# Kernel optimization log

Hardware: AMD Instinct MI355X
Metric: run time of the kernel (lower is better)

## Reference

```python
import jax, jax.numpy as jnp
import numpy as np
from jax import lax

OC, IC, K = 256, 256, 3
PAD, STRIDE = 1, 1
NNZ = 59000
N, H, W = 32, 56, 56


def setup_inputs() -> dict:
    key = jax.random.key(0)
    k1, k2, k3, k4 = jax.random.split(key, 4)
    x = jax.random.normal(k1, (N, IC, H, W), dtype=jnp.float32)
    W_val = jax.random.normal(k2, (NNZ,), dtype=jnp.float32)
    W_idx = jax.random.randint(k3, (NNZ,), 0, OC * IC * K * K, dtype=jnp.int64)
    bias = jax.random.normal(k4, (OC,), dtype=jnp.float32)
    return {"x": x, "W_val": W_val, "W_idx": W_idx, "bias": bias}


def reference(x, W_val, W_idx, bias):
    # Scatter COO values into the dense [OC, IC, K, K] weight (duplicates sum).
    dense_w = jnp.zeros((OC * IC * K * K,), dtype=W_val.dtype).at[W_idx].add(W_val)
    dense_w = dense_w.reshape(OC, IC, K, K)
    # conv2d, NCHW / OIHW layout, stride=STRIDE, symmetric padding=PAD
    out = lax.conv_general_dilated(
        x, dense_w,
        window_strides=(STRIDE, STRIDE),
        padding=[(PAD, PAD), (PAD, PAD)],
        dimension_numbers=("NCHW", "OIHW", "NCHW"),
    )
    out = out + bias[None, :, None, None]
    return out
```

## Files before the change

kernel.cpp:

```cpp
#include <hip/hip_runtime.h>

typedef unsigned short ushort;
typedef __attribute__((ext_vector_type(8))) short bf16x8;
typedef __attribute__((ext_vector_type(4))) float f32x4;
typedef __attribute__((ext_vector_type(4))) ushort us4;

#define NBATCH 32
#define ICN 256
#define OCN 256
#define HSZ 56
#define WSZ 56
#define HP 58
#define SPAT (HP*HP)
#define KTOT 2304
#define MTOT (NBATCH*HSZ*WSZ)
#define NT   (KTOT/64)

#define XP_BYTES ((size_t)NBATCH*SPAT*ICN*2)
#define WD_BYTES ((size_t)OCN*KTOT*4)
#define BM2_BYTES ((size_t)(NT+1)*2*1024*16)

__device__ __forceinline__ ushort f2bf(float f) {
  union { float f; unsigned u; } c; c.f = f;
  unsigned r = c.u + 0x7FFFu + ((c.u >> 16) & 1u);
  return (ushort)(r >> 16);
}

__global__ void k_transpose(const float* __restrict__ x, ushort* __restrict__ xp) {
  __shared__ float tile[ICN*57];
  int h = blockIdx.x, n = blockIdx.y;
  ushort* dst = xp + ((size_t)n*SPAT + (size_t)h*HP)*ICN;
  if (h == 0 || h == HP-1) {
    for (int e = threadIdx.x; e < HP*ICN/4; e += 256) ((us4*)dst)[e] = (us4){0,0,0,0};
    return;
  }
  const float* src = x + ((size_t)n*ICN*HSZ*WSZ) + (size_t)(h-1)*WSZ;
  for (int e = threadIdx.x; e < ICN*WSZ; e += 256) {
    int ic = e / WSZ, w = e - ic*WSZ;
    tile[ic*57 + w] = src[(size_t)ic*(HSZ*WSZ) + w];
  }
  __syncthreads();
  for (int e = threadIdx.x; e < ICN*HP; e += 256) {
    int w = e >> 8, ic = e & 255;
    dst[e] = (w == 0 || w == HP-1) ? (ushort)0 : f2bf(tile[ic*57 + (w-1)]);
  }
}

__global__ void k_scatter(const int* __restrict__ idx, const float* __restrict__ val,
                          float* __restrict__ wd, int nnz) {
  int i = blockIdx.x*256 + threadIdx.x;
  if (i >= nnz) return;
  int id = idx[i];
  int oc = id / (ICN*9);
  int rem = id - oc*(ICN*9);
  int ic = rem / 9;
  int k9 = rem - ic*9;
  atomicAdd(wd + (size_t)oc*KTOT + k9*ICN + ic, val[i]);
}

__global__ void k_convert2(const float* __restrict__ wd, ushort* __restrict__ bm2) {
  int e = blockIdx.x*256 + threadIdx.x;
  int t  = e >> 11;
  int kh = (e >> 10) & 1;
  int s  = e & 1023;
  int r  = s >> 2;
  int p  = s & 3;
  int o  = p ^ ((r >> 1) & 3);
  int t4 = t >> 2;
  int k  = t4*256 + ((t & 3) << 6) + (kh << 5) + o*8;
  const float* src = wd + (size_t)r*KTOT + k;
  float4 v0 = *(const float4*)(src);
  float4 v1 = *(const float4*)(src + 4);
  us4 lo, hi;
  lo[0]=f2bf(v0.x); lo[1]=f2bf(v0.y); lo[2]=f2bf(v0.z); lo[3]=f2bf(v0.w);
  hi[0]=f2bf(v1.x); hi[1]=f2bf(v1.y); hi[2]=f2bf(v1.z); hi[3]=f2bf(v1.w);
  ushort* dst = bm2 + (size_t)e*8;
  *(us4*)(dst) = lo; *(us4*)(dst+4) = hi;
}


#define GLD(gsrc, ldst) __builtin_amdgcn_global_load_lds( \
    (const __attribute__((address_space(1))) void*)(gsrc), \
    (__attribute__((address_space(3))) void*)(ldst), 16, 0, 0)
#define BAR()  asm volatile("s_barrier" ::: "memory")
#define VMW4() asm volatile("s_waitcnt vmcnt(4)" ::: "memory")
#define LGKM0 do { asm volatile("s_waitcnt lgkmcnt(0)" ::: "memory"); \
                   __builtin_amdgcn_sched_barrier(0); } while (0)
#define LGKM4 do { asm volatile("s_waitcnt lgkmcnt(4)" ::: "memory"); \
                   __builtin_amdgcn_sched_barrier(0); } while (0)
#define LGKM8 do { asm volatile("s_waitcnt lgkmcnt(8)" ::: "memory"); \
                   __builtin_amdgcn_sched_barrier(0); } while (0)

#define STAGE_AU(T1, U) do { \
    const int t4_ = (T1) >> 2; const int khh_ = t4_/3, khw_ = t4_ - khh_*3; \
    const int koff_ = (khh_*HP + khw_)*256 + (((T1) & 3) << 6); \
    ushort* d_ = &Ab[(((T1)&1)*16384) + (U)*8192]; \
    GLD(xp + ((U) ? srcA10 : srcA00) + koff_, d_ + ldsOff0); \
    GLD(xp + ((U) ? srcA11 : srcA01) + koff_, d_ + ldsOff1); } while (0)

#define STAGE_BK(T1, KH) do { \
    const ushort* s_ = bm2 + ((size_t)((T1)*2 + (KH)))*8192; \
    ushort* d_ = &Bb[(((T1)&1)*16384) + (KH)*8192]; \
    GLD(s_ + srcB0, d_ + ldsOff0); \
    GLD(s_ + srcB1, d_ + ldsOff1); } while (0)

#define LOADA_TO(DST, KH, MH, C) do { \
    unsigned a_ = ((KH) ? aL1v : aL0v) + (unsigned)((C)*32768 + (MH)*8192); \
    asm volatile("ds_read_b128 %0, %4 offset:0\n\t" \
                 "ds_read_b128 %1, %4 offset:2048\n\t" \
                 "ds_read_b128 %2, %4 offset:4096\n\t" \
                 "ds_read_b128 %3, %4 offset:6144" \
                 : "=&v"(DST[0]), "=&v"(DST[1]), "=&v"(DST[2]), "=&v"(DST[3]) \
                 : "v"(a_)); } while (0)

#define LOADB_TO(DST, KH, C) do { \
    unsigned a_ = bLv + (unsigned)((C)*32768 + (KH)*16384); \
    asm volatile("ds_read_b128 %0, %4 offset:0\n\t" \
                 "ds_read_b128 %1, %4 offset:1024\n\t" \
                 "ds_read_b128 %2, %4 offset:2048\n\t" \
                 "ds_read_b128 %3, %4 offset:3072" \
                 : "=&v"(DST[0]), "=&v"(DST[1]), "=&v"(DST[2]), "=&v"(DST[3]) \
                 : "v"(a_)); } while (0)

#define MFMA16(MH, AV, BV) do { \
    __builtin_amdgcn_s_setprio(1); \
    _Pragma("unroll") \
    for (int f_ = 0; f_ < 4; ++f_) { \
      _Pragma("unroll") \
      for (int n_ = 0; n_ < 4; ++n_) \
        acc[(MH)*4+f_][n_] = __builtin_amdgcn_mfma_f32_16x16x32_bf16( \
            AV[f_], BV[n_], acc[(MH)*4+f_][n_], 0, 0, 0); \
    } \
    __builtin_amdgcn_s_setprio(0); } while (0)

__global__ __launch_bounds__(512, 2) void k_gemm8(const ushort* __restrict__ xp,
                                                  const ushort* __restrict__ bm2,
                                                  const float* __restrict__ bias,
                                                  float* __restrict__ out) {
  __shared__ __align__(128) ushort Ab[2*2*128*64];
  __shared__ __align__(128) ushort Bb[2*2*256*32];

  const int tid = threadIdx.x;
  const int lam = tid & 63;
  const int wv  = tid >> 6;
  const int wr  = wv >> 2;
  const int wc  = wv & 3;
  const int la  = lam & 15;
  const int m0  = blockIdx.x * 256;

  const unsigned AbB = (unsigned)(uintptr_t)(__attribute__((address_space(3))) char*)Ab;
  const unsigned BbB = (unsigned)(uintptr_t)(__attribute__((address_space(3))) char*)Bb;

  const int q0 = (lam >> 4) ^ (la & 7);
  const unsigned aL0v = AbB + wr*16384 + la*128 + q0*16;
  const unsigned aL1v = AbB + wr*16384 + la*128 + (q0 ^ 4)*16;
  const int pq = (lam >> 4) ^ ((la >> 1) & 3);
  const unsigned bLv = BbB + wc*4096 + la*64 + pq*16;

  const int ldsOff0 = (0*8 + wv)*512;
  const int ldsOff1 = (1*8 + wv)*512;
  const int srcB0 = (0*8 + wv)*512 + lam*8;
  const int srcB1 = (1*8 + wv)*512 + lam*8;
  int srcA00, srcA01, srcA10, srcA11;
  {
    const int oA = (lam & 7) ^ (lam >> 3);
    int m, n, rem, oh, ow, r;
    r = (0*8 + wv)*8 + (lam >> 3);
    m = m0 + 0*128 + r; n = m/3136; rem = m - n*3136; oh = rem/56; ow = rem - oh*56;
    srcA00 = (n*SPAT + oh*HP + ow)*ICN + oA*8;
    r = (1*8 + wv)*8 + (lam >> 3);
    m = m0 + 0*128 + r; n = m/3136; rem = m - n*3136; oh = rem/56; ow = rem - oh*56;
    srcA01 = (n*SPAT + oh*HP + ow)*ICN + oA*8;
    r = (0*8 + wv)*8 + (lam >> 3);
    m = m0 + 1*128 + r; n = m/3136; rem = m - n*3136; oh = rem/56; ow = rem - oh*56;
    srcA10 = (n*SPAT + oh*HP + ow)*ICN + oA*8;
    r = (1*8 + wv)*8 + (lam >> 3);
    m = m0 + 1*128 + r; n = m/3136; rem = m - n*3136; oh = rem/56; ow = rem - oh*56;
    srcA11 = (n*SPAT + oh*HP + ow)*ICN + oA*8;
  }

  f32x4 acc[8][4];
#pragma unroll
  for (int a = 0; a < 8; ++a)
#pragma unroll
    for (int b = 0; b < 4; ++b) acc[a][b] = (f32x4){0.f, 0.f, 0.f, 0.f};

  bf16x8 av0_[4], av1_[4], bv0_[4], bv1_[4];

  STAGE_AU(0, 0); STAGE_AU(0, 1); STAGE_BK(0, 0); STAGE_BK(0, 1);
  STAGE_BK(1, 0); STAGE_BK(1, 1);
  VMW4();
  BAR();

  for (int t = 0; t < NT-1; ++t) {
    const int c = t & 1;
    LOADB_TO(bv0_, 0, c); LOADA_TO(av0_, 0, 0, c);
    STAGE_AU(t+1, 0);
    LOADA_TO(av1_, 0, 1, c);
    LGKM4;
    MFMA16(0, av0_, bv0_);
    STAGE_AU(t+1, 1);
    LOADB_TO(bv1_, 1, c); LOADA_TO(av0_, 1, 0, c);
    LGKM8;
    MFMA16(1, av1_, bv0_);
    BAR();
    STAGE_BK(t+2, 0);
    LOADA_TO(av1_, 1, 1, c);
    LGKM4;
    MFMA16(0, av0_, bv1_);
    STAGE_BK(t+2, 1);
    LGKM0;
    MFMA16(1, av1_, bv1_);
    VMW4();
    BAR();
  }

  {
    const int c = (NT-1) & 1;
    LOADB_TO(bv0_, 0, c); LOADA_TO(av0_, 0, 0, c);
    LOADA_TO(av1_, 0, 1, c);
    LGKM4;
    MFMA16(0, av0_, bv0_);
    LOADB_TO(bv1_, 1, c); LOADA_TO(av0_, 1, 0, c);
    LGKM8;
    MFMA16(1, av1_, bv0_);
    LOADA_TO(av1_, 1, 1, c);
    LGKM4;
    MFMA16(0, av0_, bv1_);
    LGKM0;
    MFMA16(1, av1_, bv1_);
  }

#pragma unroll
  for (int nn = 0; nn < 4; ++nn) {
    int oc = wc*64 + nn*16 + la;
    float bvs = bias[oc];
#pragma unroll
    for (int mf = 0; mf < 8; ++mf) {
      int m = m0 + wr*128 + mf*16 + ((lam >> 4) << 2);
      int n = m / 3136;
      int rem = m - n*3136;
      float4 o;
      o.x = acc[mf][nn][0] + bvs;
      o.y = acc[mf][nn][1] + bvs;
      o.z = acc[mf][nn][2] + bvs;
      o.w = acc[mf][nn][3] + bvs;
      *(float4*)(out + ((size_t)(n*OCN + oc))*3136 + rem) = o;
    }
  }
}

extern "C" void kernel_launch(void* const* d_in, const int* in_sizes, int n_in,
                              void* d_out, int out_size, void* d_ws, size_t ws_size,
                              hipStream_t stream) {
  const float* x    = (const float*)d_in[0];
  const float* wval = (const float*)d_in[1];
  const int*   widx = (const int*)d_in[2];
  const float* bias = (const float*)d_in[3];
  float* out = (float*)d_out;
  const int nnz = in_sizes[1];

  char* ws = (char*)d_ws;
  ushort* xp  = (ushort*)ws;
  float*  wd  = (float*)(ws + XP_BYTES);
  ushort* bm2 = (ushort*)(ws + XP_BYTES + WD_BYTES);

  hipMemsetAsync(wd, 0, WD_BYTES, stream);
  k_transpose<<<dim3(HP, NBATCH), 256, 0, stream>>>(x, xp);
  k_scatter<<<dim3((nnz + 255)/256), 256, 0, stream>>>(widx, wval, wd, nnz);
  k_convert2<<<dim3((NT*2*1024)/256), 256, 0, stream>>>(wd, bm2);
  k_gemm8<<<dim3(MTOT/256), 512, 0, stream>>>(xp, bm2, bias, out);
}
```

Before: 180.0 us.

## Load weight fragments directly from global into registers, bypassing LDS

The weight matrix is repacked by a new conversion kernel into a per-wave, per-lane MFMA fragment order, so each wave can fetch its B operands with global_load_dwordx4 straight into registers instead of staging through shared memory. This removes the B LDS buffers, their LDS reads and one barrier per iteration, and halves LDS use, which may allow more occupancy. In exchange every wave issues redundant global/L2 loads for weights and must hide their latency with vmcnt-based register double-buffering, which raises register pressure.

```diff
diff --git a/kernel.cpp b/kernel.cpp
--- a/kernel.cpp
+++ b/kernel.cpp
@@ -18,7 +18,6 @@
 
 #define XP_BYTES ((size_t)NBATCH*SPAT*ICN*2)
 #define WD_BYTES ((size_t)OCN*KTOT*4)
-#define BM2_BYTES ((size_t)(NT+1)*2*1024*16)
 
 __device__ __forceinline__ ushort f2bf(float f) {
   union { float f; unsigned u; } c; c.f = f;
@@ -58,23 +57,22 @@
   atomicAdd(wd + (size_t)oc*KTOT + k9*ICN + ic, val[i]);
 }
 
-__global__ void k_convert2(const float* __restrict__ wd, ushort* __restrict__ bm2) {
+__global__ void k_convert3(const float* __restrict__ wd, ushort* __restrict__ bm3) {
   int e = blockIdx.x*256 + threadIdx.x;
-  int t  = e >> 11;
-  int kh = (e >> 10) & 1;
-  int s  = e & 1023;
-  int r  = s >> 2;
-  int p  = s & 3;
-  int o  = p ^ ((r >> 1) & 3);
-  int t4 = t >> 2;
-  int k  = t4*256 + ((t & 3) << 6) + (kh << 5) + o*8;
-  const float* src = wd + (size_t)r*KTOT + k;
+  int lam = e & 63;
+  int f   = (e >> 6) & 3;
+  int wc  = (e >> 8) & 3;
+  int kh  = (e >> 10) & 1;
+  int t   = e >> 11;
+  int oc  = wc*64 + f*16 + (lam & 15);
+  int k   = (t >> 2)*256 + (t & 3)*64 + kh*32 + (lam >> 4)*8;
+  const float* src = wd + (size_t)oc*KTOT + k;
   float4 v0 = *(const float4*)(src);
   float4 v1 = *(const float4*)(src + 4);
   us4 lo, hi;
   lo[0]=f2bf(v0.x); lo[1]=f2bf(v0.y); lo[2]=f2bf(v0.z); lo[3]=f2bf(v0.w);
   hi[0]=f2bf(v1.x); hi[1]=f2bf(v1.y); hi[2]=f2bf(v1.z); hi[3]=f2bf(v1.w);
-  ushort* dst = bm2 + (size_t)e*8;
+  ushort* dst = bm3 + (size_t)e*8;
   *(us4*)(dst) = lo; *(us4*)(dst+4) = hi;
 }
 
@@ -83,13 +81,10 @@
     (const __attribute__((address_space(1))) void*)(gsrc), \
     (__attribute__((address_space(3))) void*)(ldst), 16, 0, 0)
 #define BAR()  asm volatile("s_barrier" ::: "memory")
-#define VMW4() asm volatile("s_waitcnt vmcnt(4)" ::: "memory")
-#define LGKM0 do { asm volatile("s_waitcnt lgkmcnt(0)" ::: "memory"); \
-                   __builtin_amdgcn_sched_barrier(0); } while (0)
-#define LGKM4 do { asm volatile("s_waitcnt lgkmcnt(4)" ::: "memory"); \
-                   __builtin_amdgcn_sched_barrier(0); } while (0)
-#define LGKM8 do { asm volatile("s_waitcnt lgkmcnt(8)" ::: "memory"); \
-                   __builtin_amdgcn_sched_barrier(0); } while (0)
+#define VMW(N) do { asm volatile("s_waitcnt vmcnt(" #N ")" ::: "memory"); \
+                    __builtin_amdgcn_sched_barrier(0); } while (0)
+#define LGKM(N) do { asm volatile("s_waitcnt lgkmcnt(" #N ")" ::: "memory"); \
+                     __builtin_amdgcn_sched_barrier(0); } while (0)
 
 #define STAGE_AU(T1, U) do { \
     const int t4_ = (T1) >> 2; const int khh_ = t4_/3, khw_ = t4_ - khh_*3; \
@@ -98,11 +93,13 @@
     GLD(xp + ((U) ? srcA10 : srcA00) + koff_, d_ + ldsOff0); \
     GLD(xp + ((U) ? srcA11 : srcA01) + koff_, d_ + ldsOff1); } while (0)
 
-#define STAGE_BK(T1, KH) do { \
-    const ushort* s_ = bm2 + ((size_t)((T1)*2 + (KH)))*8192; \
-    ushort* d_ = &Bb[(((T1)&1)*16384) + (KH)*8192]; \
-    GLD(s_ + srcB0, d_ + ldsOff0); \
-    GLD(s_ + srcB1, d_ + ldsOff1); } while (0)
+#define GLB(DST, VOFF) \
+    asm volatile("global_load_dwordx4 %0, %4, %5 offset:0\n\t" \
+                 "global_load_dwordx4 %1, %4, %5 offset:1024\n\t" \
+                 "global_load_dwordx4 %2, %4, %5 offset:2048\n\t" \
+                 "global_load_dwordx4 %3, %4, %5 offset:3072" \
+                 : "=&v"(DST[0]), "=&v"(DST[1]), "=&v"(DST[2]), "=&v"(DST[3]) \
+                 : "v"(VOFF), "s"(bm3) : "memory")
 
 #define LOADA_TO(DST, KH, MH, C) do { \
     unsigned a_ = ((KH) ? aL1v : aL0v) + (unsigned)((C)*32768 + (MH)*8192); \
@@ -110,15 +107,6 @@
                  "ds_read_b128 %1, %4 offset:2048\n\t" \
                  "ds_read_b128 %2, %4 offset:4096\n\t" \
                  "ds_read_b128 %3, %4 offset:6144" \
-                 : "=&v"(DST[0]), "=&v"(DST[1]), "=&v"(DST[2]), "=&v"(DST[3]) \
-                 : "v"(a_)); } while (0)
-
-#define LOADB_TO(DST, KH, C) do { \
-    unsigned a_ = bLv + (unsigned)((C)*32768 + (KH)*16384); \
-    asm volatile("ds_read_b128 %0, %4 offset:0\n\t" \
-                 "ds_read_b128 %1, %4 offset:1024\n\t" \
-                 "ds_read_b128 %2, %4 offset:2048\n\t" \
-                 "ds_read_b128 %3, %4 offset:3072" \
                  : "=&v"(DST[0]), "=&v"(DST[1]), "=&v"(DST[2]), "=&v"(DST[3]) \
                  : "v"(a_)); } while (0)
 
@@ -134,11 +122,10 @@
     __builtin_amdgcn_s_setprio(0); } while (0)
 
 __global__ __launch_bounds__(512, 2) void k_gemm8(const ushort* __restrict__ xp,
-                                                  const ushort* __restrict__ bm2,
+                                                  const ushort* __restrict__ bm3,
                                                   const float* __restrict__ bias,
                                                   float* __restrict__ out) {
   __shared__ __align__(128) ushort Ab[2*2*128*64];
-  __shared__ __align__(128) ushort Bb[2*2*256*32];
 
   const int tid = threadIdx.x;
   const int lam = tid & 63;
@@ -149,18 +136,15 @@
   const int m0  = blockIdx.x * 256;
 
   const unsigned AbB = (unsigned)(uintptr_t)(__attribute__((address_space(3))) char*)Ab;
-  const unsigned BbB = (unsigned)(uintptr_t)(__attribute__((address_space(3))) char*)Bb;
 
   const int q0 = (lam >> 4) ^ (la & 7);
   const unsigned aL0v = AbB + wr*16384 + la*128 + q0*16;
   const unsigned aL1v = AbB + wr*16384 + la*128 + (q0 ^ 4)*16;
-  const int pq = (lam >> 4) ^ ((la >> 1) & 3);
-  const unsigned bLv = BbB + wc*4096 + la*64 + pq*16;
+
+  const unsigned wcB = wc*4096 + lam*16;
 
   const int ldsOff0 = (0*8 + wv)*512;
   const int ldsOff1 = (1*8 + wv)*512;
-  const int srcB0 = (0*8 + wv)*512 + lam*8;
-  const int srcB1 = (1*8 + wv)*512 + lam*8;
   int srcA00, srcA01, srcA10, srcA11;
   {
     const int oA = (lam & 7) ^ (lam >> 3);
@@ -185,50 +169,54 @@
 #pragma unroll
     for (int b = 0; b < 4; ++b) acc[a][b] = (f32x4){0.f, 0.f, 0.f, 0.f};
 
-  bf16x8 av0_[4], av1_[4], bv0_[4], bv1_[4];
-
-  STAGE_AU(0, 0); STAGE_AU(0, 1); STAGE_BK(0, 0); STAGE_BK(0, 1);
-  STAGE_BK(1, 0); STAGE_BK(1, 1);
-  VMW4();
+  bf16x8 av0_[4], av1_[4], bvA_[4], bvB_[4];
+
+  STAGE_AU(0, 0); STAGE_AU(0, 1);
+  GLB(bvA_, wcB);
+  VMW(4);
   BAR();
 
   for (int t = 0; t < NT-1; ++t) {
     const int c = t & 1;
-    LOADB_TO(bv0_, 0, c); LOADA_TO(av0_, 0, 0, c);
+    const unsigned vb = (unsigned)t*32768 + wcB;
+    GLB(bvB_, vb + 16384);
     STAGE_AU(t+1, 0);
-    LOADA_TO(av1_, 0, 1, c);
-    LGKM4;
-    MFMA16(0, av0_, bv0_);
+    LOADA_TO(av0_, 0, 0, c); LOADA_TO(av1_, 0, 1, c);
+    VMW(6);
+    LGKM(4);
+    MFMA16(0, av0_, bvA_);
     STAGE_AU(t+1, 1);
-    LOADB_TO(bv1_, 1, c); LOADA_TO(av0_, 1, 0, c);
-    LGKM8;
-    MFMA16(1, av1_, bv0_);
-    BAR();
-    STAGE_BK(t+2, 0);
+    LOADA_TO(av0_, 1, 0, c);
+    LGKM(4);
+    MFMA16(1, av1_, bvA_);
+    GLB(bvA_, vb + 32768);
     LOADA_TO(av1_, 1, 1, c);
-    LGKM4;
-    MFMA16(0, av0_, bv1_);
-    STAGE_BK(t+2, 1);
-    LGKM0;
-    MFMA16(1, av1_, bv1_);
-    VMW4();
+    VMW(8);
+    LGKM(4);
+    MFMA16(0, av0_, bvB_);
+    LGKM(0);
+    MFMA16(1, av1_, bvB_);
+    VMW(4);
     BAR();
   }
 
   {
     const int c = (NT-1) & 1;
-    LOADB_TO(bv0_, 0, c); LOADA_TO(av0_, 0, 0, c);
-    LOADA_TO(av1_, 0, 1, c);
-    LGKM4;
-    MFMA16(0, av0_, bv0_);
-    LOADB_TO(bv1_, 1, c); LOADA_TO(av0_, 1, 0, c);
-    LGKM8;
-    MFMA16(1, av1_, bv0_);
+    const unsigned vb = (unsigned)(NT-1)*32768 + wcB;
+    GLB(bvB_, vb + 16384);
+    LOADA_TO(av0_, 0, 0, c); LOADA_TO(av1_, 0, 1, c);
+    VMW(4);
+    LGKM(4);
+    MFMA16(0, av0_, bvA_);
+    LOADA_TO(av0_, 1, 0, c);
+    LGKM(4);
+    MFMA16(1, av1_, bvA_);
     LOADA_TO(av1_, 1, 1, c);
-    LGKM4;
-    MFMA16(0, av0_, bv1_);
-    LGKM0;
-    MFMA16(1, av1_, bv1_);
+    VMW(0);
+    LGKM(4);
+    MFMA16(0, av0_, bvB_);
+    LGKM(0);
+    MFMA16(1, av1_, bvB_);
   }
 
 #pragma unroll
@@ -263,11 +251,11 @@
   char* ws = (char*)d_ws;
   ushort* xp  = (ushort*)ws;
   float*  wd  = (float*)(ws + XP_BYTES);
-  ushort* bm2 = (ushort*)(ws + XP_BYTES + WD_BYTES);
+  ushort* bm3 = (ushort*)(ws + XP_BYTES + WD_BYTES);
 
   hipMemsetAsync(wd, 0, WD_BYTES, stream);
   k_transpose<<<dim3(HP, NBATCH), 256, 0, stream>>>(x, xp);
   k_scatter<<<dim3((nnz + 255)/256), 256, 0, stream>>>(widx, wval, wd, nnz);
-  k_convert2<<<dim3((NT*2*1024)/256), 256, 0, stream>>>(wd, bm2);
-  k_gemm8<<<dim3(MTOT/256), 512, 0, stream>>>(xp, bm2, bias, out);
-}
+  k_convert3<<<dim3((NT*2*16*64)/256), 256, 0, stream>>>(wd, bm3);
+  k_gemm8<<<dim3(MTOT/256), 512, 0, stream>>>(xp, bm3, bias, out);
+}
```

Measured after the change: 177.1 us. About the same (-1.6%).
